# Kernel tuning notes

Measured on AMD Instinct MI355X. Metric: run time of the kernel, lower is better.

## Reference

```python
import jax, jax.numpy as jnp
import numpy as np

K = 1024   # codebook size
C = 8      # codebook channels
D = K // C # per-channel code dim = 128
BETA = 0.25
B = 8192   # batch of latent vectors, each of size C*D = K


def setup_inputs() -> dict:
    key = jax.random.key(0)
    k1, k2, k3 = jax.random.split(key, 3)
    latents = jax.random.normal(k1, (B, C * D), dtype=jnp.float32)
    # nn.Embedding(K, D) init: uniform(-1/K, 1/K)
    embedding = jax.random.uniform(k2, (K, D), dtype=jnp.float32,
                                   minval=-1.0 / K, maxval=1.0 / K)
    k = jax.random.randint(k3, (C,), 0, 8, dtype=jnp.int32)
    return {"latents": latents, "embedding": embedding, "k": k}


def reference(latents, embedding, k):
    sg = jax.lax.stop_gradient
    flat = latents.reshape(-1, D)                                  # [B*C, D]
    # squared euclidean distance to every code: [B*C, K]
    dist = (jnp.sum(flat ** 2, axis=1, keepdims=True)
            + jnp.sum(embedding ** 2, axis=1)
            - 2.0 * (flat @ embedding.T))
    order = jnp.argsort(dist, axis=1).reshape(-1, C, K)            # [B, C, K]
    # per channel c, pick the k[c]-th nearest code index
    sel = jnp.take_along_axis(order, k[None, :, None], axis=2)[..., 0]  # [B, C]
    # one-hot @ embedding == plain gather of selected rows
    quantized = embedding[sel.reshape(-1)].reshape(latents.shape)  # [B, C*D]
    commitment_loss = jnp.mean((sg(quantized) - latents) ** 2)
    embedding_loss = jnp.mean((quantized - sg(latents)) ** 2)
    vq_loss = BETA * commitment_loss + embedding_loss
    # straight-through estimator
    quantized_st = latents + sg(quantized - latents)
    return quantized_st, vq_loss
```

## Files before the change

### kernel.cpp

```cpp
#include <hip/hip_runtime.h>

#define KDIM   128
#define NELEM  8388608

typedef __attribute__((ext_vector_type(4))) float f32x4;
typedef __attribute__((ext_vector_type(2))) int   int2v;

__device__ inline f32x4 mfma8(long long a, long long b, f32x4 c) {
  return __builtin_amdgcn_mfma_f32_16x16x32_fp8_fp8(a, b, c, 0, 0, 0);
}
__device__ inline void gload16(const void* g, void* l) {
  __builtin_amdgcn_global_load_lds(
      (const __attribute__((address_space(1))) unsigned*)g,
      (__attribute__((address_space(3))) unsigned*)l, 16, 0, 0);
}
__device__ inline long long pk8(float4 v0, float4 v1) {
  int lo = __builtin_amdgcn_cvt_pk_fp8_f32(v0.x, v0.y, 0, false);
  lo     = __builtin_amdgcn_cvt_pk_fp8_f32(v0.z, v0.w, lo, true);
  int hi = __builtin_amdgcn_cvt_pk_fp8_f32(v1.x, v1.y, 0, false);
  hi     = __builtin_amdgcn_cvt_pk_fp8_f32(v1.z, v1.w, hi, true);
  int2v t; t.x = lo; t.y = hi;
  return __builtin_bit_cast(long long, t);
}
__device__ inline float packk(float s, int c) {
  return __builtin_bit_cast(float,
      (__builtin_bit_cast(unsigned, s) & 0xFFFFFC00u) | (unsigned)c);
}
__device__ inline float sumsq(float4 a, float4 b) {
  return a.x*a.x + a.y*a.y + a.z*a.z + a.w*a.w + b.x*b.x + b.y*b.y + b.z*b.z + b.w*b.w;
}
__device__ inline void merge8(float (&t)[8], int msk) {
  float o[8];
#pragma unroll
  for (int p = 0; p < 8; ++p) o[p] = __shfl_xor(t[p], msk);
  float m[8];
#pragma unroll
  for (int p = 0; p < 8; ++p) m[p] = fmaxf(t[p], o[7 - p]);
#pragma unroll
  for (int s = 4; s; s >>= 1)
#pragma unroll
    for (int i = 0; i < 8; ++i)
      if (!(i & s)) {
        float x = fmaxf(m[i], m[i | s]);
        m[i | s] = fminf(m[i], m[i | s]);
        m[i] = x;
      }
#pragma unroll
  for (int p = 0; p < 8; ++p) t[p] = m[p];
}

__global__ void vq_prep(const float* __restrict__ emb, unsigned char* __restrict__ ebf8,
                        float* __restrict__ esqm, unsigned long long* __restrict__ lossAcc,
                        unsigned* __restrict__ cnt) {
  int j = blockIdx.x, d = threadIdx.x;
  float v = emb[j * KDIM + d];
  float vs = v * 1024.0f;
  int p = __builtin_amdgcn_cvt_pk_fp8_f32(vs, vs, 0, false);
  ebf8[j * KDIM + (d ^ ((j & 15) << 3))] = (unsigned char)(p & 0xFF);
  float s = v * v;
#pragma unroll
  for (int m = 1; m <= 32; m <<= 1) s += __shfl_xor(s, m);
  __shared__ float w[2];
  if ((d & 63) == 0) w[d >> 6] = s;
  __syncthreads();
  if (d == 0) esqm[j] = -512.0f * (w[0] + w[1]);
  if (j == 0 && d == 0) { lossAcc[0] = 0ULL; cnt[0] = 0u; }
}

__device__ inline void scan_codes(const unsigned char* bk0, const unsigned char* bk1,
                                  const unsigned char* bk2, const unsigned char* bk3,
                                  const float* esqmLds, int hi,
                                  long long v0, long long v1, long long v2, long long v3,
                                  float (&top)[8]) {
  int cid = hi * 4;
#pragma unroll 4
  for (int pp = 0; pp < 32; ++pp) {
    const int off = pp * 4096;
    const float* eb = esqmLds + pp * 32 + hi * 4;
    f32x4 a0 = *(const f32x4*)(eb);
    f32x4 a1 = *(const f32x4*)(eb + 16);
    a0 = mfma8(*(const long long*)(bk0 + off), v0, a0);
    a0 = mfma8(*(const long long*)(bk1 + off), v1, a0);
    a0 = mfma8(*(const long long*)(bk2 + off), v2, a0);
    a0 = mfma8(*(const long long*)(bk3 + off), v3, a0);
    a1 = mfma8(*(const long long*)(bk0 + off + 2048), v0, a1);
    a1 = mfma8(*(const long long*)(bk1 + off + 2048), v1, a1);
    a1 = mfma8(*(const long long*)(bk2 + off + 2048), v2, a1);
    a1 = mfma8(*(const long long*)(bk3 + off + 2048), v3, a1);
    float k0 = packk(a0[0], cid + 0),  k1 = packk(a0[1], cid + 1);
    float k2 = packk(a0[2], cid + 2),  k3 = packk(a0[3], cid + 3);
    float k4 = packk(a1[0], cid + 16), k5 = packk(a1[1], cid + 17);
    float k6 = packk(a1[2], cid + 18), k7 = packk(a1[3], cid + 19);
    float x = fmaxf(fmaxf(fmaxf(k0, k1), fmaxf(k2, k3)),
                    fmaxf(fmaxf(k4, k5), fmaxf(k6, k7)));
#pragma unroll
    for (int p = 0; p < 8; ++p) {
      float mx = fmaxf(top[p], x);
      x = fminf(top[p], x);
      top[p] = mx;
    }
    cid += 32;
  }
}

__device__ inline void write_rows(const float* __restrict__ emb, float* __restrict__ outp,
                                  int grow0, int idx, int lane) {
#pragma unroll 4
  for (int r = 0; r < 16; ++r) {
    int s2 = __shfl(idx, r);
    float2 qv = *(const float2*)(emb + (size_t)s2 * KDIM + lane * 2);
    *(float2*)(outp + (size_t)(grow0 + r) * KDIM + lane * 2) = qv;
  }
}

__global__ __launch_bounds__(512, 1) void vq_main(
    const float* __restrict__ lat, const float* __restrict__ emb,
    const int* __restrict__ ksel, const unsigned char* __restrict__ ebf8,
    const float* __restrict__ esqm, float* __restrict__ out,
    unsigned long long* __restrict__ lossAcc, unsigned* __restrict__ cnt,
    float* __restrict__ loss) {
  __shared__ __align__(16) unsigned char smem[131072 + 4096 + 64];
  float* esqmLds = (float*)(smem + 131072);
  float* wLds    = (float*)(smem + 131072 + 4096);

  const int tid = threadIdx.x, lane = tid & 63, wid = tid >> 6;
  const int n = lane & 15, hi = lane >> 4;
  const int gR0 = blockIdx.x * 256;

  const float* rp0 = lat + (size_t)(gR0 + wid * 32 + n) * KDIM + hi * 8;
  float4 p0[4], p1[4];
#pragma unroll
  for (int ks = 0; ks < 4; ++ks) {
    p0[ks] = *(const float4*)(rp0 + ks * 32);
    p1[ks] = *(const float4*)(rp0 + ks * 32 + 4);
  }
  {
    const char* src = (const char*)ebf8 + tid * 16;
    char* dst = (char*)smem + tid * 16;
#pragma unroll
    for (int qq = 0; qq < 16; ++qq) gload16(src + qq * 8192, dst + qq * 8192);
    if (tid < 256) gload16((const char*)esqm + tid * 16, (char*)esqmLds + tid * 16);
  }
  const float* rp1 = rp0 + 16 * KDIM;
  float4 q0[4], q1[4];
#pragma unroll
  for (int ks = 0; ks < 4; ++ks) {
    q0[ks] = *(const float4*)(rp1 + ks * 32);
    q1[ks] = *(const float4*)(rp1 + ks * 32 + 4);
  }
  float fsq0;
  long long b00, b01, b02, b03;
  {
    float s = 0.f;
#pragma unroll
    for (int ks = 0; ks < 4; ++ks) s += sumsq(p0[ks], p1[ks]);
    s += __shfl_xor(s, 16); s += __shfl_xor(s, 32);
    fsq0 = s;
    b00 = pk8(p0[0], p1[0]); b01 = pk8(p0[1], p1[1]);
    b02 = pk8(p0[2], p1[2]); b03 = pk8(p0[3], p1[3]);
  }
  asm volatile("s_waitcnt vmcnt(0)" ::: "memory");
  __builtin_amdgcn_s_barrier();

  const unsigned char* ab = smem + n * 128 + ((hi ^ (n & 3)) << 3);
  const int nh = n >> 2;
  const unsigned char* bk0 = ab + ((0 ^ nh) << 5);
  const unsigned char* bk1 = ab + ((1 ^ nh) << 5);
  const unsigned char* bk2 = ab + ((2 ^ nh) << 5);
  const unsigned char* bk3 = ab + ((3 ^ nh) << 5);

  const float NINF = __builtin_bit_cast(float, 0xFF800000u);
  float top0[8], top1[8];
#pragma unroll
  for (int p = 0; p < 8; ++p) { top0[p] = NINF; top1[p] = NINF; }

  scan_codes(bk0, bk1, bk2, bk3, esqmLds, hi, b00, b01, b02, b03, top0);

  float fsq1;
  long long b10, b11, b12, b13;
  {
    float s = 0.f;
#pragma unroll
    for (int ks = 0; ks < 4; ++ks) s += sumsq(q0[ks], q1[ks]);
    s += __shfl_xor(s, 16); s += __shfl_xor(s, 32);
    fsq1 = s;
    b10 = pk8(q0[0], q1[0]); b11 = pk8(q0[1], q1[1]);
    b12 = pk8(q0[2], q1[2]); b13 = pk8(q0[3], q1[3]);
  }

  int kk = ksel[lane & 7];
  kk = kk < 0 ? 0 : (kk > 7 ? 7 : kk);

  merge8(top0, 16); merge8(top0, 32);
  float sel0 = top0[0];
#pragma unroll
  for (int p = 1; p < 8; ++p) sel0 = (kk == p) ? top0[p] : sel0;
  unsigned sb0 = __builtin_bit_cast(unsigned, sel0);
  int idx0 = (int)(sb0 & 1023u);
  float rl0 = fsq0 - __builtin_bit_cast(float, sb0 & 0xFFFFFC00u) * (1.0f / 512.0f);
  write_rows(emb, out, gR0 + wid * 32, idx0, lane);

  scan_codes(bk0, bk1, bk2, bk3, esqmLds, hi, b10, b11, b12, b13, top1);
  merge8(top1, 16); merge8(top1, 32);
  float sel1 = top1[0];
#pragma unroll
  for (int p = 1; p < 8; ++p) sel1 = (kk == p) ? top1[p] : sel1;
  unsigned sb1 = __builtin_bit_cast(unsigned, sel1);
  int idx1 = (int)(sb1 & 1023u);
  float rl1 = fsq1 - __builtin_bit_cast(float, sb1 & 0xFFFFFC00u) * (1.0f / 512.0f);
  write_rows(emb, out, gR0 + wid * 32 + 16, idx1, lane);

  float c = (lane < 16) ? (rl0 + rl1) : 0.f;
#pragma unroll
  for (int m = 1; m <= 32; m <<= 1) c += __shfl_xor(c, m);
  if (lane == 0) wLds[wid] = c;
  __syncthreads();
  if (tid == 0) {
    double bs = 0.0;
#pragma unroll
    for (int w = 0; w < 8; ++w) bs += (double)wLds[w];
    long long iv = (long long)(bs * 1048576.0 + 0.5);
    atomicAdd(lossAcc, (unsigned long long)iv);
    __threadfence();
    unsigned done = atomicAdd(cnt, 1u);
    if (done == 255u) {
      unsigned long long tot = atomicAdd(lossAcc, 0ULL);
      loss[0] = (float)((double)(long long)tot * (1.25 / (1048576.0 * 8388608.0)));
    }
  }
}

extern "C" void kernel_launch(void* const* d_in, const int* in_sizes, int n_in,
                              void* d_out, int out_size, void* d_ws, size_t ws_size,
                              hipStream_t stream) {
  const float* lat = (const float*)d_in[0];
  const float* emb = (const float*)d_in[1];
  const int* ksel = (const int*)d_in[2];
  float* out = (float*)d_out;

  unsigned char* ebf8 = (unsigned char*)d_ws;
  float* esqm = (float*)((char*)d_ws + 131072);
  unsigned long long* lossAcc =
      (unsigned long long*)((char*)d_ws + 135168);
  unsigned* cnt = (unsigned*)((char*)d_ws + 135176);

  vq_prep<<<1024, 128, 0, stream>>>(emb, ebf8, esqm, lossAcc, cnt);
  vq_main<<<256, 512, 0, stream>>>(lat, emb, ksel, ebf8, esqm, out, lossAcc, cnt,
                                   out + NELEM);
}
```

Before: 47.20 us.

## Double waves per block so each wave scans one 16-row tile

Blocks grow from 512 to 1024 threads. Each wave now processes one 16-row group instead of two sequential groups, which removes the second code scan per wave and its prefetch registers. The MFMA accumulation is split into two independent chains per output tile and summed afterwards to shorten the dependency chain, and the scan unroll drops from 4 to 2. The launch bound of (1024, 4) asks for far more resident waves than the 130 KB LDS per block allows, so it may cap VGPRs tightly and cause spills.

```diff
diff --git a/kernel.cpp b/kernel.cpp
--- a/kernel.cpp
+++ b/kernel.cpp
@@ -73,20 +73,24 @@
                                   long long v0, long long v1, long long v2, long long v3,
                                   float (&top)[8]) {
   int cid = hi * 4;
-#pragma unroll 4
+#pragma unroll 2
   for (int pp = 0; pp < 32; ++pp) {
     const int off = pp * 4096;
     const float* eb = esqmLds + pp * 32 + hi * 4;
     f32x4 a0 = *(const f32x4*)(eb);
     f32x4 a1 = *(const f32x4*)(eb + 16);
+    f32x4 c0 = (f32x4){0.f, 0.f, 0.f, 0.f};
+    f32x4 c1 = (f32x4){0.f, 0.f, 0.f, 0.f};
     a0 = mfma8(*(const long long*)(bk0 + off), v0, a0);
     a0 = mfma8(*(const long long*)(bk1 + off), v1, a0);
-    a0 = mfma8(*(const long long*)(bk2 + off), v2, a0);
-    a0 = mfma8(*(const long long*)(bk3 + off), v3, a0);
+    c0 = mfma8(*(const long long*)(bk2 + off), v2, c0);
+    c0 = mfma8(*(const long long*)(bk3 + off), v3, c0);
     a1 = mfma8(*(const long long*)(bk0 + off + 2048), v0, a1);
     a1 = mfma8(*(const long long*)(bk1 + off + 2048), v1, a1);
-    a1 = mfma8(*(const long long*)(bk2 + off + 2048), v2, a1);
-    a1 = mfma8(*(const long long*)(bk3 + off + 2048), v3, a1);
+    c1 = mfma8(*(const long long*)(bk2 + off + 2048), v2, c1);
+    c1 = mfma8(*(const long long*)(bk3 + off + 2048), v3, c1);
+    a0 += c0;
+    a1 += c1;
     float k0 = packk(a0[0], cid + 0),  k1 = packk(a0[1], cid + 1);
     float k2 = packk(a0[2], cid + 2),  k3 = packk(a0[3], cid + 3);
     float k4 = packk(a1[0], cid + 16), k5 = packk(a1[1], cid + 17);
@@ -113,7 +117,7 @@
   }
 }
 
-__global__ __launch_bounds__(512, 1) void vq_main(
+__global__ __launch_bounds__(1024, 4) void vq_main(
     const float* __restrict__ lat, const float* __restrict__ emb,
     const int* __restrict__ ksel, const unsigned char* __restrict__ ebf8,
     const float* __restrict__ esqm, float* __restrict__ out,
@@ -127,7 +131,7 @@
   const int n = lane & 15, hi = lane >> 4;
   const int gR0 = blockIdx.x * 256;
 
-  const float* rp0 = lat + (size_t)(gR0 + wid * 32 + n) * KDIM + hi * 8;
+  const float* rp0 = lat + (size_t)(gR0 + wid * 16 + n) * KDIM + hi * 8;
   float4 p0[4], p1[4];
 #pragma unroll
   for (int ks = 0; ks < 4; ++ks) {
@@ -138,15 +142,8 @@
     const char* src = (const char*)ebf8 + tid * 16;
     char* dst = (char*)smem + tid * 16;
 #pragma unroll
-    for (int qq = 0; qq < 16; ++qq) gload16(src + qq * 8192, dst + qq * 8192);
+    for (int qq = 0; qq < 8; ++qq) gload16(src + qq * 16384, dst + qq * 16384);
     if (tid < 256) gload16((const char*)esqm + tid * 16, (char*)esqmLds + tid * 16);
-  }
-  const float* rp1 = rp0 + 16 * KDIM;
-  float4 q0[4], q1[4];
-#pragma unroll
-  for (int ks = 0; ks < 4; ++ks) {
-    q0[ks] = *(const float4*)(rp1 + ks * 32);
-    q1[ks] = *(const float4*)(rp1 + ks * 32 + 4);
   }
   float fsq0;
   long long b00, b01, b02, b03;
@@ -170,23 +167,11 @@
   const unsigned char* bk3 = ab + ((3 ^ nh) << 5);
 
   const float NINF = __builtin_bit_cast(float, 0xFF800000u);
-  float top0[8], top1[8];
-#pragma unroll
-  for (int p = 0; p < 8; ++p) { top0[p] = NINF; top1[p] = NINF; }
+  float top0[8];
+#pragma unroll
+  for (int p = 0; p < 8; ++p) top0[p] = NINF;
 
   scan_codes(bk0, bk1, bk2, bk3, esqmLds, hi, b00, b01, b02, b03, top0);
-
-  float fsq1;
-  long long b10, b11, b12, b13;
-  {
-    float s = 0.f;
-#pragma unroll
-    for (int ks = 0; ks < 4; ++ks) s += sumsq(q0[ks], q1[ks]);
-    s += __shfl_xor(s, 16); s += __shfl_xor(s, 32);
-    fsq1 = s;
-    b10 = pk8(q0[0], q1[0]); b11 = pk8(q0[1], q1[1]);
-    b12 = pk8(q0[2], q1[2]); b13 = pk8(q0[3], q1[3]);
-  }
 
   int kk = ksel[lane & 7];
   kk = kk < 0 ? 0 : (kk > 7 ? 7 : kk);
@@ -198,19 +183,9 @@
   unsigned sb0 = __builtin_bit_cast(unsigned, sel0);
   int idx0 = (int)(sb0 & 1023u);
   float rl0 = fsq0 - __builtin_bit_cast(float, sb0 & 0xFFFFFC00u) * (1.0f / 512.0f);
-  write_rows(emb, out, gR0 + wid * 32, idx0, lane);
-
-  scan_codes(bk0, bk1, bk2, bk3, esqmLds, hi, b10, b11, b12, b13, top1);
-  merge8(top1, 16); merge8(top1, 32);
-  float sel1 = top1[0];
-#pragma unroll
-  for (int p = 1; p < 8; ++p) sel1 = (kk == p) ? top1[p] : sel1;
-  unsigned sb1 = __builtin_bit_cast(unsigned, sel1);
-  int idx1 = (int)(sb1 & 1023u);
-  float rl1 = fsq1 - __builtin_bit_cast(float, sb1 & 0xFFFFFC00u) * (1.0f / 512.0f);
-  write_rows(emb, out, gR0 + wid * 32 + 16, idx1, lane);
-
-  float c = (lane < 16) ? (rl0 + rl1) : 0.f;
+  write_rows(emb, out, gR0 + wid * 16, idx0, lane);
+
+  float c = (lane < 16) ? rl0 : 0.f;
 #pragma unroll
   for (int m = 1; m <= 32; m <<= 1) c += __shfl_xor(c, m);
   if (lane == 0) wLds[wid] = c;
@@ -218,7 +193,7 @@
   if (tid == 0) {
     double bs = 0.0;
 #pragma unroll
-    for (int w = 0; w < 8; ++w) bs += (double)wLds[w];
+    for (int w = 0; w < 16; ++w) bs += (double)wLds[w];
     long long iv = (long long)(bs * 1048576.0 + 0.5);
     atomicAdd(lossAcc, (unsigned long long)iv);
     __threadfence();
@@ -245,6 +220,6 @@
   unsigned* cnt = (unsigned*)((char*)d_ws + 135176);
 
   vq_prep<<<1024, 128, 0, stream>>>(emb, ebf8, esqm, lossAcc, cnt);
-  vq_main<<<256, 512, 0, stream>>>(lat, emb, ksel, ebf8, esqm, out, lossAcc, cnt,
-                                   out + NELEM);
-}
+  vq_main<<<256, 1024, 0, stream>>>(lat, emb, ksel, ebf8, esqm, out, lossAcc, cnt,
+                                    out + NELEM);
+}
```

Result: faster. 44.20 us (-6.4%).

## Fuse two row-group code scans into one loop sharing LDS codebook loads

Applied to the files above, without the earlier changes.

The two sequential scans over the 1024-code FP8 codebook, one per 16-row group, become a single loop. Each LDS fragment and esqm bias is loaded once and fed to four independent MFMA accumulator chains, which halves LDS reads and gives more instruction-level parallelism. The loop start is also rotated per wave (stw = wid*4) to spread LDS bank and address traffic across waves. In exchange, register pressure rises (both sets of operands, two top-8 lists and four accumulators stay live), and the second group's row writes no longer overlap with the second scan.

```diff
diff --git a/kernel.cpp b/kernel.cpp
--- a/kernel.cpp
+++ b/kernel.cpp
@@ -47,6 +47,14 @@
       }
 #pragma unroll
   for (int p = 0; p < 8; ++p) t[p] = m[p];
+}
+__device__ inline void ins8(float (&top)[8], float x) {
+#pragma unroll
+  for (int p = 0; p < 8; ++p) {
+    float mx = fmaxf(top[p], x);
+    x = fminf(top[p], x);
+    top[p] = mx;
+  }
 }
 
 __global__ void vq_prep(const float* __restrict__ emb, unsigned char* __restrict__ ebf8,
@@ -67,42 +75,6 @@
   if (j == 0 && d == 0) { lossAcc[0] = 0ULL; cnt[0] = 0u; }
 }
 
-__device__ inline void scan_codes(const unsigned char* bk0, const unsigned char* bk1,
-                                  const unsigned char* bk2, const unsigned char* bk3,
-                                  const float* esqmLds, int hi,
-                                  long long v0, long long v1, long long v2, long long v3,
-                                  float (&top)[8]) {
-  int cid = hi * 4;
-#pragma unroll 4
-  for (int pp = 0; pp < 32; ++pp) {
-    const int off = pp * 4096;
-    const float* eb = esqmLds + pp * 32 + hi * 4;
-    f32x4 a0 = *(const f32x4*)(eb);
-    f32x4 a1 = *(const f32x4*)(eb + 16);
-    a0 = mfma8(*(const long long*)(bk0 + off), v0, a0);
-    a0 = mfma8(*(const long long*)(bk1 + off), v1, a0);
-    a0 = mfma8(*(const long long*)(bk2 + off), v2, a0);
-    a0 = mfma8(*(const long long*)(bk3 + off), v3, a0);
-    a1 = mfma8(*(const long long*)(bk0 + off + 2048), v0, a1);
-    a1 = mfma8(*(const long long*)(bk1 + off + 2048), v1, a1);
-    a1 = mfma8(*(const long long*)(bk2 + off + 2048), v2, a1);
-    a1 = mfma8(*(const long long*)(bk3 + off + 2048), v3, a1);
-    float k0 = packk(a0[0], cid + 0),  k1 = packk(a0[1], cid + 1);
-    float k2 = packk(a0[2], cid + 2),  k3 = packk(a0[3], cid + 3);
-    float k4 = packk(a1[0], cid + 16), k5 = packk(a1[1], cid + 17);
-    float k6 = packk(a1[2], cid + 18), k7 = packk(a1[3], cid + 19);
-    float x = fmaxf(fmaxf(fmaxf(k0, k1), fmaxf(k2, k3)),
-                    fmaxf(fmaxf(k4, k5), fmaxf(k6, k7)));
-#pragma unroll
-    for (int p = 0; p < 8; ++p) {
-      float mx = fmaxf(top[p], x);
-      x = fminf(top[p], x);
-      top[p] = mx;
-    }
-    cid += 32;
-  }
-}
-
 __device__ inline void write_rows(const float* __restrict__ emb, float* __restrict__ outp,
                                   int grow0, int idx, int lane) {
 #pragma unroll 4
@@ -128,11 +100,14 @@
   const int gR0 = blockIdx.x * 256;
 
   const float* rp0 = lat + (size_t)(gR0 + wid * 32 + n) * KDIM + hi * 8;
-  float4 p0[4], p1[4];
+  const float* rp1 = rp0 + 16 * KDIM;
+  float4 p0[4], p1[4], q0[4], q1[4];
 #pragma unroll
   for (int ks = 0; ks < 4; ++ks) {
     p0[ks] = *(const float4*)(rp0 + ks * 32);
     p1[ks] = *(const float4*)(rp0 + ks * 32 + 4);
+    q0[ks] = *(const float4*)(rp1 + ks * 32);
+    q1[ks] = *(const float4*)(rp1 + ks * 32 + 4);
   }
   {
     const char* src = (const char*)ebf8 + tid * 16;
@@ -141,23 +116,22 @@
     for (int qq = 0; qq < 16; ++qq) gload16(src + qq * 8192, dst + qq * 8192);
     if (tid < 256) gload16((const char*)esqm + tid * 16, (char*)esqmLds + tid * 16);
   }
-  const float* rp1 = rp0 + 16 * KDIM;
-  float4 q0[4], q1[4];
-#pragma unroll
-  for (int ks = 0; ks < 4; ++ks) {
-    q0[ks] = *(const float4*)(rp1 + ks * 32);
-    q1[ks] = *(const float4*)(rp1 + ks * 32 + 4);
-  }
-  float fsq0;
-  long long b00, b01, b02, b03;
+  float fsq0, fsq1;
+  long long b00, b01, b02, b03, b10, b11, b12, b13;
   {
-    float s = 0.f;
-#pragma unroll
-    for (int ks = 0; ks < 4; ++ks) s += sumsq(p0[ks], p1[ks]);
-    s += __shfl_xor(s, 16); s += __shfl_xor(s, 32);
-    fsq0 = s;
+    float s0 = 0.f, s1 = 0.f;
+#pragma unroll
+    for (int ks = 0; ks < 4; ++ks) {
+      s0 += sumsq(p0[ks], p1[ks]);
+      s1 += sumsq(q0[ks], q1[ks]);
+    }
+    s0 += __shfl_xor(s0, 16); s0 += __shfl_xor(s0, 32);
+    s1 += __shfl_xor(s1, 16); s1 += __shfl_xor(s1, 32);
+    fsq0 = s0; fsq1 = s1;
     b00 = pk8(p0[0], p1[0]); b01 = pk8(p0[1], p1[1]);
     b02 = pk8(p0[2], p1[2]); b03 = pk8(p0[3], p1[3]);
+    b10 = pk8(q0[0], q1[0]); b11 = pk8(q0[1], q1[1]);
+    b12 = pk8(q0[2], q1[2]); b13 = pk8(q0[3], q1[3]);
   }
   asm volatile("s_waitcnt vmcnt(0)" ::: "memory");
   __builtin_amdgcn_s_barrier();
@@ -174,18 +148,51 @@
 #pragma unroll
   for (int p = 0; p < 8; ++p) { top0[p] = NINF; top1[p] = NINF; }
 
-  scan_codes(bk0, bk1, bk2, bk3, esqmLds, hi, b00, b01, b02, b03, top0);
-
-  float fsq1;
-  long long b10, b11, b12, b13;
-  {
-    float s = 0.f;
-#pragma unroll
-    for (int ks = 0; ks < 4; ++ks) s += sumsq(q0[ks], q1[ks]);
-    s += __shfl_xor(s, 16); s += __shfl_xor(s, 32);
-    fsq1 = s;
-    b10 = pk8(q0[0], q1[0]); b11 = pk8(q0[1], q1[1]);
-    b12 = pk8(q0[2], q1[2]); b13 = pk8(q0[3], q1[3]);
+  const int stw = wid * 4;
+#pragma unroll 4
+  for (int pp = 0; pp < 32; ++pp) {
+    const int g = (pp + stw) & 31;
+    const int off = g * 4096;
+    const float* eb = esqmLds + g * 32 + hi * 4;
+    f32x4 e0 = *(const f32x4*)(eb);
+    f32x4 e1 = *(const f32x4*)(eb + 16);
+    long long t0 = *(const long long*)(bk0 + off);
+    long long t1 = *(const long long*)(bk1 + off);
+    long long t2 = *(const long long*)(bk2 + off);
+    long long t3 = *(const long long*)(bk3 + off);
+    long long u0 = *(const long long*)(bk0 + off + 2048);
+    long long u1 = *(const long long*)(bk1 + off + 2048);
+    long long u2 = *(const long long*)(bk2 + off + 2048);
+    long long u3 = *(const long long*)(bk3 + off + 2048);
+    f32x4 a0 = e0, a1 = e1, a2 = e0, a3 = e1;
+    a0 = mfma8(t0, b00, a0); a1 = mfma8(u0, b00, a1);
+    a2 = mfma8(t0, b10, a2); a3 = mfma8(u0, b10, a3);
+    a0 = mfma8(t1, b01, a0); a1 = mfma8(u1, b01, a1);
+    a2 = mfma8(t1, b11, a2); a3 = mfma8(u1, b11, a3);
+    a0 = mfma8(t2, b02, a0); a1 = mfma8(u2, b02, a1);
+    a2 = mfma8(t2, b12, a2); a3 = mfma8(u2, b12, a3);
+    a0 = mfma8(t3, b03, a0); a1 = mfma8(u3, b03, a1);
+    a2 = mfma8(t3, b13, a2); a3 = mfma8(u3, b13, a3);
+
+    const int cb = g * 32 + hi * 4;
+    {
+      float k0 = packk(a0[0], cb + 0),  k1 = packk(a0[1], cb + 1);
+      float k2 = packk(a0[2], cb + 2),  k3 = packk(a0[3], cb + 3);
+      float k4 = packk(a1[0], cb + 16), k5 = packk(a1[1], cb + 17);
+      float k6 = packk(a1[2], cb + 18), k7 = packk(a1[3], cb + 19);
+      float x = fmaxf(fmaxf(fmaxf(k0, k1), fmaxf(k2, k3)),
+                      fmaxf(fmaxf(k4, k5), fmaxf(k6, k7)));
+      ins8(top0, x);
+    }
+    {
+      float k0 = packk(a2[0], cb + 0),  k1 = packk(a2[1], cb + 1);
+      float k2 = packk(a2[2], cb + 2),  k3 = packk(a2[3], cb + 3);
+      float k4 = packk(a3[0], cb + 16), k5 = packk(a3[1], cb + 17);
+      float k6 = packk(a3[2], cb + 18), k7 = packk(a3[3], cb + 19);
+      float x = fmaxf(fmaxf(fmaxf(k0, k1), fmaxf(k2, k3)),
+                      fmaxf(fmaxf(k4, k5), fmaxf(k6, k7)));
+      ins8(top1, x);
+    }
   }
 
   int kk = ksel[lane & 7];
@@ -200,7 +207,6 @@
   float rl0 = fsq0 - __builtin_bit_cast(float, sb0 & 0xFFFFFC00u) * (1.0f / 512.0f);
   write_rows(emb, out, gR0 + wid * 32, idx0, lane);
 
-  scan_codes(bk0, bk1, bk2, bk3, esqmLds, hi, b10, b11, b12, b13, top1);
   merge8(top1, 16); merge8(top1, 32);
   float sel1 = top1[0];
 #pragma unroll
```

Result: faster. 44.85 us (-5.0%).
